# Optimization experiments

Hardware: AMD Instinct MI355X
Metric: run time of the kernel (lower is better)

Reference implementation:

```python
import jax, jax.numpy as jnp
import numpy as np

D_MODEL = 1024
NUM_HEADS = 16
D_K = D_MODEL // NUM_HEADS


def setup_inputs() -> dict:
    key = jax.random.key(0)
    kx, kq, kk, kv, ko = jax.random.split(key, 5)
    B, S = 4, 2048
    scale = 1.0 / np.sqrt(D_MODEL)
    return {
        "x": jax.random.normal(kx, (B, S, D_MODEL), dtype=jnp.float32),
        "W_q": jax.random.normal(kq, (D_MODEL, D_MODEL), dtype=jnp.float32) * scale,
        "W_k": jax.random.normal(kk, (D_MODEL, D_MODEL), dtype=jnp.float32) * scale,
        "W_v": jax.random.normal(kv, (D_MODEL, D_MODEL), dtype=jnp.float32) * scale,
        "W_o": jax.random.normal(ko, (D_MODEL, D_MODEL), dtype=jnp.float32) * scale,
    }


def reference(x, W_q, W_k, W_v, W_o):
    B, S, _ = x.shape
    # torch Linear: y = x @ W.T
    def proj(W):
        return (x @ W.T).reshape(B, S, NUM_HEADS, D_K).transpose(0, 2, 1, 3)  # [B,H,S,Dk]
    Q, K, V = proj(W_q), proj(W_k), proj(W_v)
    scores = jnp.einsum("bhqd,bhkd->bhqk", Q, K) / jnp.sqrt(jnp.float32(D_K))
    attn = jax.nn.softmax(scores, axis=-1)
    out = jnp.einsum("bhqk,bhkd->bhqd", attn, V)  # [B,H,S,Dk]
    out = out.transpose(0, 2, 1, 3).reshape(B, S, D_MODEL)
    return out @ W_o.T
```

## Files before the change

kernel.cpp:

```cpp
#include <hip/hip_runtime.h>
#include <hip/hip_bf16.h>

typedef unsigned short u16;
typedef __bf16 bf16x8 __attribute__((ext_vector_type(8)));
typedef float f32x4 __attribute__((ext_vector_type(4)));

#define DEV static __device__ __forceinline__

DEV u16 f2b(float f){
  union { float f; unsigned u; } v; v.f = f;
  unsigned r = (v.u + 0x7FFFu + ((v.u >> 16) & 1u)) >> 16;
  return (u16)r;
}

DEV unsigned pack2(float lo, float hi){
  __hip_bfloat162 h = __float22bfloat162_rn(float2{lo, hi});
  union { __hip_bfloat162 h; unsigned u; } c; c.h = h;
  return c.u;
}

DEV unsigned pack_trunc(float lo, float hi){
  union { float f; unsigned u; } a, b; a.f = lo; b.f = hi;
  return __builtin_amdgcn_perm(b.u, a.u, 0x07060302u);
}

DEV void gload16(const void* g, void* l){
  __builtin_amdgcn_global_load_lds((const __attribute__((address_space(1))) void*)g,
                                   (__attribute__((address_space(3))) void*)l, 16, 0, 0);
}

DEV f32x4 mfma16(bf16x8 a, bf16x8 b, f32x4 c){
  return __builtin_amdgcn_mfma_f32_16x16x32_bf16(a, b, c, 0, 0, 0);
}

__global__ void cvt_kernel(const float* __restrict__ src, u16* __restrict__ dst, int n4){
  int i = blockIdx.x * 256 + threadIdx.x;
  if (i < n4){
    float4 v = reinterpret_cast<const float4*>(src)[i];
    ushort4 o;
    o.x = f2b(v.x); o.y = f2b(v.y); o.z = f2b(v.z); o.w = f2b(v.w);
    reinterpret_cast<ushort4*>(dst)[i] = o;
  }
}

__global__ void cvt4_kernel(const float* __restrict__ w0, const float* __restrict__ w1,
                            const float* __restrict__ w2, const float* __restrict__ w3,
                            u16* __restrict__ o0, u16* __restrict__ o1,
                            u16* __restrict__ o2, u16* __restrict__ o3){
  int r = blockIdx.x >> 10;
  int i = (blockIdx.x & 1023) * 256 + threadIdx.x;
  const float* s = (r == 0) ? w0 : (r == 1) ? w1 : (r == 2) ? w2 : w3;
  u16*         d = (r == 0) ? o0 : (r == 1) ? o1 : (r == 2) ? o2 : o3;
  float4 v = reinterpret_cast<const float4*>(s)[i];
  ushort4 o;
  o.x = f2b(v.x); o.y = f2b(v.y); o.z = f2b(v.z); o.w = f2b(v.w);
  reinterpret_cast<ushort4*>(d)[i] = o;
}

__global__ __launch_bounds__(256, 2)
void gemm_qkv(const u16* __restrict__ A, const u16* __restrict__ B,
              u16* __restrict__ Qb, u16* __restrict__ Kb, u16* __restrict__ Vtb){
  __shared__ __align__(16) u16 lsA[128*64];
  __shared__ __align__(16) u16 lsB[128*64];
  const int tid  = threadIdx.x;
  const int lane = tid & 63, wid = tid >> 6;
  const int g = lane >> 4, c15 = lane & 15;
  const int m0 = blockIdx.x * 128, n0 = blockIdx.y * 128;
  const int wm = (wid >> 1) * 64, wn = (wid & 1) * 64;
  const f32x4 vzero = {0.f, 0.f, 0.f, 0.f};

  f32x4 acc[4][4];
#pragma unroll
  for (int mi = 0; mi < 4; ++mi)
#pragma unroll
    for (int ni = 0; ni < 4; ++ni) acc[mi][ni] = vzero;

  for (int kt = 0; kt < 16; ++kt){
    __syncthreads();
#pragma unroll
    for (int i = 0; i < 4; ++i){
      int c = i * 256 + tid;
      int row = c >> 3, gc = (c & 7) ^ (row & 7);
      gload16(A + ((size_t)(m0 + row) << 10) + (kt << 6) + (gc << 3), lsA + (size_t)c * 8);
    }
#pragma unroll
    for (int i = 0; i < 4; ++i){
      int c = i * 256 + tid;
      int row = c >> 3, gc = (c & 7) ^ (row & 7);
      gload16(B + ((size_t)(n0 + row) << 10) + (kt << 6) + (gc << 3), lsB + (size_t)c * 8);
    }
    __syncthreads();

    bf16x8 af[4][2], bf[4][2];
#pragma unroll
    for (int mi = 0; mi < 4; ++mi)
#pragma unroll
      for (int kk = 0; kk < 2; ++kk){
        int ra = wm + mi * 16 + c15;
        af[mi][kk] = *reinterpret_cast<const bf16x8*>(lsA + ra * 64 + ((((kk << 2) + g) ^ (ra & 7)) << 3));
        int rb = wn + mi * 16 + c15;
        bf[mi][kk] = *reinterpret_cast<const bf16x8*>(lsB + rb * 64 + ((((kk << 2) + g) ^ (rb & 7)) << 3));
      }
#pragma unroll
    for (int mi = 0; mi < 4; ++mi)
#pragma unroll
      for (int ni = 0; ni < 4; ++ni){
        acc[mi][ni] = mfma16(af[mi][0], bf[ni][0], acc[mi][ni]);
        acc[mi][ni] = mfma16(af[mi][1], bf[ni][1], acc[mi][ni]);
      }
  }

  const int reg = n0 >> 10;
#pragma unroll
  for (int mi = 0; mi < 4; ++mi)
#pragma unroll
    for (int ni = 0; ni < 4; ++ni){
      int mrow = m0 + wm + mi * 16 + g * 4;
      int ncolL = (n0 + wn + ni * 16 + c15) & 1023;
      int b = mrow >> 11, s = mrow & 2047;
      int h = ncolL >> 6, dk = ncolL & 63;
      if (reg < 2){
        const float sc = (reg == 0) ? 0.125f : 1.0f;
        u16* dst = (reg == 0 ? Qb : Kb) + (((size_t)(b * 16 + h) * 2048 + s) << 6) + dk;
#pragma unroll
        for (int r = 0; r < 4; ++r) dst[(size_t)r << 6] = f2b(acc[mi][ni][r] * sc);
      } else {
        ushort4 o;
        o.x = f2b(acc[mi][ni][0]); o.y = f2b(acc[mi][ni][1]);
        o.z = f2b(acc[mi][ni][2]); o.w = f2b(acc[mi][ni][3]);
        *reinterpret_cast<ushort4*>(Vtb + (((size_t)(b * 16 + h) * 64 + dk) << 11) + s) = o;
      }
    }
}

__global__ __launch_bounds__(256, 2)
void gemm_out(const u16* __restrict__ A, const u16* __restrict__ B, float* __restrict__ Out){
  __shared__ __align__(16) u16 lsA[128*64];
  __shared__ __align__(16) u16 lsB[128*64];
  const int tid  = threadIdx.x;
  const int lane = tid & 63, wid = tid >> 6;
  const int g = lane >> 4, c15 = lane & 15;
  const int m0 = blockIdx.x * 128, n0 = blockIdx.y * 128;
  const int wm = (wid >> 1) * 64, wn = (wid & 1) * 64;
  const f32x4 vzero = {0.f, 0.f, 0.f, 0.f};

  f32x4 acc[4][4];
#pragma unroll
  for (int mi = 0; mi < 4; ++mi)
#pragma unroll
    for (int ni = 0; ni < 4; ++ni) acc[mi][ni] = vzero;

  for (int kt = 0; kt < 16; ++kt){
    __syncthreads();
#pragma unroll
    for (int i = 0; i < 4; ++i){
      int c = i * 256 + tid;
      int row = c >> 3, gc = (c & 7) ^ (row & 7);
      int b = m0 >> 11, s = (m0 & 2047) + row;
      gload16(A + (((size_t)(b * 16 + kt) * 2048 + s) << 6) + (gc << 3), lsA + (size_t)c * 8);
    }
#pragma unroll
    for (int i = 0; i < 4; ++i){
      int c = i * 256 + tid;
      int row = c >> 3, gc = (c & 7) ^ (row & 7);
      gload16(B + ((size_t)(n0 + row) << 10) + (kt << 6) + (gc << 3), lsB + (size_t)c * 8);
    }
    __syncthreads();

    bf16x8 af[4][2], bf[4][2];
#pragma unroll
    for (int mi = 0; mi < 4; ++mi)
#pragma unroll
      for (int kk = 0; kk < 2; ++kk){
        int ra = wm + mi * 16 + c15;
        af[mi][kk] = *reinterpret_cast<const bf16x8*>(lsA + ra * 64 + ((((kk << 2) + g) ^ (ra & 7)) << 3));
        int rb = wn + mi * 16 + c15;
        bf[mi][kk] = *reinterpret_cast<const bf16x8*>(lsB + rb * 64 + ((((kk << 2) + g) ^ (rb & 7)) << 3));
      }
#pragma unroll
    for (int mi = 0; mi < 4; ++mi)
#pragma unroll
      for (int ni = 0; ni < 4; ++ni){
        acc[mi][ni] = mfma16(af[mi][0], bf[ni][0], acc[mi][ni]);
        acc[mi][ni] = mfma16(af[mi][1], bf[ni][1], acc[mi][ni]);
      }
  }

#pragma unroll
  for (int mi = 0; mi < 4; ++mi)
#pragma unroll
    for (int ni = 0; ni < 4; ++ni){
      int mrow = m0 + wm + mi * 16 + g * 4;
      int ncol = n0 + wn + ni * 16 + c15;
      float* dst = Out + (size_t)mrow * 1024 + ncol;
#pragma unroll
      for (int r = 0; r < 4; ++r) dst[(size_t)r << 10] = acc[mi][ni][r];
    }
}

__global__ __launch_bounds__(256, 4)
void attn_kernel(const u16* __restrict__ Q, const u16* __restrict__ K,
                 const u16* __restrict__ Vt, u16* __restrict__ O){
  __shared__ __align__(16) u16 lsK[2][64*64];
  __shared__ __align__(16) u16 lsV[2][64*64];
  const int tid  = threadIdx.x;
  const int lane = tid & 63;
  const int g = lane >> 4, c15 = lane & 15;
  const int bid  = blockIdx.x;
  const int head = (bid & 7) * 8 + ((bid >> 3) >> 4);
  const int qt   = (bid >> 3) & 15;
  const size_t hb = (size_t)head << 17;
  const int q0 = qt * 128 + (tid >> 6) * 32;
  const f32x4 vzero = {0.f, 0.f, 0.f, 0.f};

  const int srcA = c15 + ((lane & 16) << 1);
  const int srcB = srcA + 16;
  const bool hihalf = (lane >= 32);

#define STAGE_T(tb, tt) do {                                                        \
    _Pragma("unroll")                                                               \
    for (int i_ = 0; i_ < 2; ++i_){                                                 \
      int c_ = i_ * 256 + tid;                                                      \
      int row_ = c_ >> 3, gc_ = (c_ & 7) ^ (row_ & 7);                              \
      gload16(K  + hb + ((size_t)((tt)*64 + row_) << 6) + (gc_ << 3), lsK[tb] + (size_t)c_ * 8); \
      gload16(Vt + hb + ((size_t)row_ << 11) + (tt)*64 + (gc_ << 3),  lsV[tb] + (size_t)c_ * 8); \
    }                                                                               \
  } while (0)

  bf16x8 qf[2][2];
#pragma unroll
  for (int mi = 0; mi < 2; ++mi)
#pragma unroll
    for (int kk = 0; kk < 2; ++kk)
      qf[mi][kk] = *reinterpret_cast<const bf16x8*>(Q + hb + ((size_t)(q0 + mi*16 + c15) << 6) + kk*32 + g*8);

  union { unsigned u[4]; bf16x8 v; } ou;
  ou.u[0] = ou.u[1] = ou.u[2] = ou.u[3] = 0x3F803F80u;
  const bf16x8 ones = ou.v;

  f32x4 oaccT[2][4];
  float mrun[2], lrun[2];
#pragma unroll
  for (int mi = 0; mi < 2; ++mi){
#pragma unroll
    for (int di = 0; di < 4; ++di) oaccT[mi][di] = vzero;
    mrun[mi] = -1e30f; lrun[mi] = 0.f;
  }

  STAGE_T(0, 0);
  __syncthreads();

  for (int t = 0; t < 32; ++t){
    const int cur = t & 1;
    if (t < 31) STAGE_T(cur ^ 1, t + 1);
    const u16* bK = lsK[cur];
    const u16* bV = lsV[cur];

    bf16x8 kf[4][2];
#pragma unroll
    for (int ni = 0; ni < 4; ++ni)
#pragma unroll
      for (int kk = 0; kk < 2; ++kk){
        int row = ni*16 + c15;
        kf[ni][kk] = *reinterpret_cast<const bf16x8*>(bK + row*64 + ((((kk<<2)+g) ^ (row&7)) << 3));
      }
    f32x4 sacc[2][4];
    __builtin_amdgcn_s_setprio(1);
#pragma unroll
    for (int mi = 0; mi < 2; ++mi)
#pragma unroll
      for (int ni = 0; ni < 4; ++ni)
        sacc[mi][ni] = mfma16(kf[ni][1], qf[mi][1], mfma16(kf[ni][0], qf[mi][0], vzero));
    __builtin_amdgcn_s_setprio(0);

    unsigned pk[2][4][2];
#pragma unroll
    for (int mi = 0; mi < 2; ++mi){
      float a0 = fmaxf(fmaxf(sacc[mi][0][0], sacc[mi][0][1]), sacc[mi][0][2]);
      float a1 = fmaxf(fmaxf(sacc[mi][0][3], sacc[mi][1][0]), sacc[mi][1][1]);
      float a2 = fmaxf(fmaxf(sacc[mi][1][2], sacc[mi][1][3]), sacc[mi][2][0]);
      float a3 = fmaxf(fmaxf(sacc[mi][2][1], sacc[mi][2][2]), sacc[mi][2][3]);
      float a4 = fmaxf(fmaxf(sacc[mi][3][0], sacc[mi][3][1]), sacc[mi][3][2]);
      float b0 = fmaxf(fmaxf(a0, a1), a2);
      float b1 = fmaxf(fmaxf(a3, a4), sacc[mi][3][3]);
      float mt = fmaxf(b0, b1);
      mt = fmaxf(mt, __shfl_xor(mt, 16, 64));
      mt = fmaxf(mt, __shfl_xor(mt, 32, 64));
      if (mt > mrun[mi]){
        float f_ = __expf(mrun[mi] - mt);
        mrun[mi] = mt;
        lrun[mi] *= f_;
#pragma unroll
        for (int di = 0; di < 4; ++di) oaccT[mi][di] = oaccT[mi][di] * f_;
      }
      const float mn = mrun[mi];
#pragma unroll
      for (int ni = 0; ni < 4; ++ni){
        float p0 = __expf(sacc[mi][ni][0] - mn);
        float p1 = __expf(sacc[mi][ni][1] - mn);
        float p2 = __expf(sacc[mi][ni][2] - mn);
        float p3 = __expf(sacc[mi][ni][3] - mn);
        pk[mi][ni][0] = pack_trunc(p0, p1);
        pk[mi][ni][1] = pack_trunc(p2, p3);
      }
    }

    bf16x8 pf[2][2];
#pragma unroll
    for (int mi = 0; mi < 2; ++mi)
#pragma unroll
      for (int kk = 0; kk < 2; ++kk){
        union { unsigned u[4]; bf16x8 v; } pu;
#pragma unroll
        for (int w = 0; w < 4; ++w){
          const int p = w & 1;
          const int src = (w < 2) ? srcA : srcB;
          unsigned va = (unsigned)__shfl((int)pk[mi][2*kk    ][p], src, 64);
          unsigned vb = (unsigned)__shfl((int)pk[mi][2*kk + 1][p], src, 64);
          pu.u[w] = hihalf ? vb : va;
        }
        pf[mi][kk] = pu.v;
      }

    bf16x8 vf[4][2];
#pragma unroll
    for (int di = 0; di < 4; ++di)
#pragma unroll
      for (int kk = 0; kk < 2; ++kk){
        int row = di*16 + c15;
        vf[di][kk] = *reinterpret_cast<const bf16x8*>(bV + row*64 + ((((kk<<2)+g) ^ (row&7)) << 3));
      }

    __builtin_amdgcn_s_setprio(1);
#pragma unroll
    for (int mi = 0; mi < 2; ++mi){
      f32x4 ls = mfma16(ones, pf[mi][0], vzero);
      ls = mfma16(ones, pf[mi][1], ls);
      lrun[mi] += ls[0];
    }
#pragma unroll
    for (int mi = 0; mi < 2; ++mi)
#pragma unroll
      for (int di = 0; di < 4; ++di){
        oaccT[mi][di] = mfma16(vf[di][0], pf[mi][0], oaccT[mi][di]);
        oaccT[mi][di] = mfma16(vf[di][1], pf[mi][1], oaccT[mi][di]);
      }
    __builtin_amdgcn_s_setprio(0);

    __syncthreads();
  }

#pragma unroll
  for (int mi = 0; mi < 2; ++mi){
    float inv = 1.f / lrun[mi];
    int q = q0 + mi*16 + c15;
#pragma unroll
    for (int di = 0; di < 4; ++di){
      unsigned lo = pack2(oaccT[mi][di][0] * inv, oaccT[mi][di][1] * inv);
      unsigned hi = pack2(oaccT[mi][di][2] * inv, oaccT[mi][di][3] * inv);
      *reinterpret_cast<uint2*>(O + hb + ((size_t)q << 6) + di*16 + g*4) = make_uint2(lo, hi);
    }
  }
#undef STAGE_T
}

extern "C" void kernel_launch(void* const* d_in, const int* in_sizes, int n_in,
                              void* d_out, int out_size, void* d_ws, size_t ws_size,
                              hipStream_t stream){
  const float* x  = (const float*)d_in[0];
  const float* wq = (const float*)d_in[1];
  const float* wk = (const float*)d_in[2];
  const float* wv = (const float*)d_in[3];
  const float* wo = (const float*)d_in[4];
  float* out = (float*)d_out;
  char* ws = (char*)d_ws;
  u16* xb  = (u16*)(ws);
  u16* wqb = (u16*)(ws + (16u << 20));
  u16* wkb = (u16*)(ws + (18u << 20));
  u16* wvb = (u16*)(ws + (20u << 20));
  u16* wob = (u16*)(ws + (22u << 20));
  u16* Qb  = (u16*)(ws + (24u << 20));
  u16* Kb  = (u16*)(ws + (40u << 20));
  u16* Vtb = (u16*)(ws + (56u << 20));
  u16* Ob  = (u16*)(ws + (72u << 20));

  cvt_kernel<<<8192, 256, 0, stream>>>(x, xb, 2097152);
  cvt4_kernel<<<4096, 256, 0, stream>>>(wq, wk, wv, wo, wqb, wkb, wvb, wob);
  gemm_qkv<<<dim3(64, 24), 256, 0, stream>>>(xb, wqb, Qb, Kb, Vtb);
  attn_kernel<<<1024, 256, 0, stream>>>(Qb, Kb, Vtb, Ob);
  gemm_out<<<dim3(64, 8), 256, 0, stream>>>(Ob, wob, out);
}
```

Measured before the change: 203.3 us.

## Load K/V fragments directly from global memory instead of LDS staging

```diff
diff --git a/kernel.cpp b/kernel.cpp
--- a/kernel.cpp
+++ b/kernel.cpp
@@ -201,8 +201,6 @@
 __global__ __launch_bounds__(256, 4)
 void attn_kernel(const u16* __restrict__ Q, const u16* __restrict__ K,
                  const u16* __restrict__ Vt, u16* __restrict__ O){
-  __shared__ __align__(16) u16 lsK[2][64*64];
-  __shared__ __align__(16) u16 lsV[2][64*64];
   const int tid  = threadIdx.x;
   const int lane = tid & 63;
   const int g = lane >> 4, c15 = lane & 15;
@@ -217,15 +215,8 @@
   const int srcB = srcA + 16;
   const bool hihalf = (lane >= 32);
 
-#define STAGE_T(tb, tt) do {                                                        \
-    _Pragma("unroll")                                                               \
-    for (int i_ = 0; i_ < 2; ++i_){                                                 \
-      int c_ = i_ * 256 + tid;                                                      \
-      int row_ = c_ >> 3, gc_ = (c_ & 7) ^ (row_ & 7);                              \
-      gload16(K  + hb + ((size_t)((tt)*64 + row_) << 6) + (gc_ << 3), lsK[tb] + (size_t)c_ * 8); \
-      gload16(Vt + hb + ((size_t)row_ << 11) + (tt)*64 + (gc_ << 3),  lsV[tb] + (size_t)c_ * 8); \
-    }                                                                               \
-  } while (0)
+  const u16* Kf = K  + hb + ((size_t)c15 << 6)  + g * 8;
+  const u16* Vf = Vt + hb + ((size_t)c15 << 11) + g * 8;
 
   bf16x8 qf[2][2];
 #pragma unroll
@@ -247,23 +238,14 @@
     mrun[mi] = -1e30f; lrun[mi] = 0.f;
   }
 
-  STAGE_T(0, 0);
-  __syncthreads();
-
   for (int t = 0; t < 32; ++t){
-    const int cur = t & 1;
-    if (t < 31) STAGE_T(cur ^ 1, t + 1);
-    const u16* bK = lsK[cur];
-    const u16* bV = lsV[cur];
-
     bf16x8 kf[4][2];
 #pragma unroll
     for (int ni = 0; ni < 4; ++ni)
 #pragma unroll
-      for (int kk = 0; kk < 2; ++kk){
-        int row = ni*16 + c15;
-        kf[ni][kk] = *reinterpret_cast<const bf16x8*>(bK + row*64 + ((((kk<<2)+g) ^ (row&7)) << 3));
-      }
+      for (int kk = 0; kk < 2; ++kk)
+        kf[ni][kk] = *reinterpret_cast<const bf16x8*>(Kf + ((size_t)(t*64 + ni*16) << 6) + kk*32);
+
     f32x4 sacc[2][4];
     __builtin_amdgcn_s_setprio(1);
 #pragma unroll
@@ -272,6 +254,13 @@
       for (int ni = 0; ni < 4; ++ni)
         sacc[mi][ni] = mfma16(kf[ni][1], qf[mi][1], mfma16(kf[ni][0], qf[mi][0], vzero));
     __builtin_amdgcn_s_setprio(0);
+
+    bf16x8 vf[4][2];
+#pragma unroll
+    for (int di = 0; di < 4; ++di)
+#pragma unroll
+      for (int kk = 0; kk < 2; ++kk)
+        vf[di][kk] = *reinterpret_cast<const bf16x8*>(Vf + ((size_t)(di*16) << 11) + t*64 + kk*32);
 
     unsigned pk[2][4][2];
 #pragma unroll
@@ -322,15 +311,6 @@
         pf[mi][kk] = pu.v;
       }
 
-    bf16x8 vf[4][2];
-#pragma unroll
-    for (int di = 0; di < 4; ++di)
-#pragma unroll
-      for (int kk = 0; kk < 2; ++kk){
-        int row = di*16 + c15;
-        vf[di][kk] = *reinterpret_cast<const bf16x8*>(bV + row*64 + ((((kk<<2)+g) ^ (row&7)) << 3));
-      }
-
     __builtin_amdgcn_s_setprio(1);
 #pragma unroll
     for (int mi = 0; mi < 2; ++mi){
@@ -346,8 +326,6 @@
         oaccT[mi][di] = mfma16(vf[di][1], pf[mi][1], oaccT[mi][di]);
       }
     __builtin_amdgcn_s_setprio(0);
-
-    __syncthreads();
   }
 
 #pragma unroll
@@ -361,7 +339,6 @@
       *reinterpret_cast<uint2*>(O + hb + ((size_t)q << 6) + di*16 + g*4) = make_uint2(lo, hi);
     }
   }
-#undef STAGE_T
 }
 
 extern "C" void kernel_launch(void* const* d_in, const int* in_sizes, int n_in,
```

Result: slower. 342.5 us (+68.5%).
